# Optimization experiments

Hardware: AMD Instinct MI355X
Metric: run time of the kernel (lower is better)

The kernel has to match this reference:

```python
import jax, jax.numpy as jnp
import numpy as np

T, NTOK, D = 8, 32768, 128
N_ENTIRE, COMP_LEN, COMP_DIM = 65536, 8, 64


def _layer_norm(v, w, b, eps=1e-5):
    m = v.mean(-1, keepdims=True)
    c = v - m
    var = (c * c).mean(-1, keepdims=True)
    return c * jax.lax.rsqrt(var + eps) * w + b


def setup_inputs() -> dict:
    key = jax.random.key(0)
    ks = jax.random.split(key, 8)
    x = jax.random.normal(ks[0], (T, NTOK, D), jnp.float32)
    padded_node_mask = jnp.ones((T, NTOK), dtype=bool)  # all tokens are nodes
    # unique per-timestamp scatter indices into the 'entire node' axis
    node_idx = jax.vmap(lambda k: jax.random.permutation(k, N_ENTIRE)[:NTOK])(
        jax.random.split(ks[1], T)).astype(jnp.int32)
    s = 0.02
    return dict(
        x=x,
        ln1_w=jnp.ones((D,), jnp.float32), ln1_b=jnp.zeros((D,), jnp.float32),
        w1=jax.random.normal(ks[2], (D, 2 * COMP_DIM), jnp.float32) * s,
        b1=jnp.zeros((2 * COMP_DIM,), jnp.float32),
        w2=jax.random.normal(ks[3], (2 * COMP_DIM, COMP_DIM), jnp.float32) * s,
        b2=jnp.zeros((COMP_DIM,), jnp.float32),
        lnf_w=jnp.ones((COMP_LEN * COMP_DIM,), jnp.float32),
        lnf_b=jnp.zeros((COMP_LEN * COMP_DIM,), jnp.float32),
        padded_node_mask=padded_node_mask,
        node_idx=node_idx,
        n_entire=N_ENTIRE,
    )


def reference(x, ln1_w, ln1_b, w1, b1, w2, b2, lnf_w, lnf_b,
              padded_node_mask, node_idx, n_entire):
    t, ntok, d = x.shape
    # encode_layer_norm over all tokens
    xn = _layer_norm(x, ln1_w, ln1_b)
    # nodes = xn[padded_node_mask].reshape(t, ntok, d); mask is all-True here
    nodes = jnp.where(padded_node_mask[..., None], xn, 0.0)
    # scga._to_entire: scatter nodes into [t, n_entire, d] (zeros elsewhere)
    tenodes = jnp.zeros((t, n_entire, d), x.dtype)
    tenodes = tenodes.at[jnp.arange(t)[:, None], node_idx].set(nodes)
    # eval mode: np.array_split(arange(n_entire), comp_len) = equal contiguous groups
    g = n_entire // COMP_LEN
    xg = tenodes.reshape(t, COMP_LEN, g, d)  # [t, L, g, d]
    # per-group MLP (Linear->GELU->(Dropout=id)->Linear) then mean over group
    h = jax.nn.gelu(jnp.einsum('tlgd,de->tlge', xg, w1) + b1, approximate=False)
    c = jnp.einsum('tlge,ec->tlgc', h, w2) + b2
    comp = c.mean(axis=2)  # [t, L, comp_dim]
    compressed = _layer_norm(comp.reshape(t, 1, COMP_LEN * COMP_DIM), lnf_w, lnf_b)
    # orthogonality loss over the L compressed components (exact torch pair loop)
    f = comp.transpose(1, 0, 2).reshape(COMP_LEN, -1)  # [L, t*comp_dim]
    fn = f / jnp.linalg.norm(f, axis=-1, keepdims=True)
    dots = []
    for i in range(COMP_LEN - 1):
        for j in range(1, COMP_LEN):
            dots.append(jnp.sum(fn[i] * fn[j]) / jnp.sum(fn[i] + fn[j]))
    ortho_loss = jnp.mean(jnp.stack(dots) ** 2)
    return compressed, ortho_loss
```

## Files before the change

### kernel.cpp

```cpp
#include <hip/hip_runtime.h>
#include <math.h>

#define TT 8
#define NTOK 32768
#define DD 128
#define LCOMP 8
#define GSZ 8192
#define CDIM 64
#define EDIM 128
#define NPART 32

#define TOKB 64
#define NBLK (TT*NTOK/TOKB)

#define O_CZERO 0
#define O_W2BT  256
#define O_W1BT  (256 + EDIM*CDIM*2)
#define O_CSUMP (O_W1BT + DD*EDIM*2)

typedef __attribute__((ext_vector_type(8))) short bf16x8;
typedef __attribute__((ext_vector_type(4))) float f32x4;

__device__ __forceinline__ ushort f2bf(float f) {
    union { float f; uint u; } c; c.f = f;
    uint u = c.u;
    return (ushort)((u + 0x7FFFu + ((u >> 16) & 1u)) >> 16);
}

__device__ __forceinline__ float gelu_f(float a) {
    float x = a * 0.70710678118654752f;
    float ax = fabsf(x);
    float t = 1.0f / (1.0f + 0.3275911f * ax);
    float p = t * (0.254829592f + t * (-0.284496736f + t * (1.421413741f +
              t * (-1.453152027f + t * 1.061405429f))));
    float e = __expf(-x * x);
    float er = copysignf(1.0f - p * e, x);
    return 0.5f * a * (1.0f + er);
}

__device__ __forceinline__ void gl_lds16(const void* g, void* l) {
    __builtin_amdgcn_global_load_lds(
        (const __attribute__((address_space(1))) void*)g,
        (__attribute__((address_space(3))) void*)l, 16, 0, 0);
}

__global__ void prep_kernel(const float* __restrict__ w1, const float* __restrict__ b1,
                            const float* __restrict__ w2,
                            ushort* __restrict__ w1bt, ushort* __restrict__ w2bt,
                            float* __restrict__ czero) {
    int gid = blockIdx.x * 256 + threadIdx.x;
    if (gid < DD * EDIM) {
        int j = gid >> 7, d = gid & 127;
        int slot = (d >> 3) ^ (j & 7);
        w1bt[j * 128 + slot * 8 + (d & 7)] = f2bf(w1[d * EDIM + j]);
    }
    if (gid < EDIM * CDIM) {
        int k = gid >> 7, jj = gid & 127;
        w2bt[k * 128 + jj] = f2bf(w2[jj * CDIM + k]);
    }
    if (gid < CDIM) {
        float a2 = 0.f;
        for (int dd = 0; dd < EDIM; ++dd)
            a2 += gelu_f(b1[dd]) * w2[dd * CDIM + gid];
        czero[gid] = a2;
    }
}

__global__ __launch_bounds__(256, 2)
void main_kernel(const float* __restrict__ x,
                 const float* __restrict__ ln1w, const float* __restrict__ ln1b,
                 const float* __restrict__ b1g,
                 const ushort* __restrict__ w1bt, const ushort* __restrict__ w2bt,
                 const float* __restrict__ czero,
                 const int* __restrict__ node_idx,
                 float* __restrict__ csum_p) {
    __shared__ float  s_x[TOKB * DD];
    __shared__ ushort s_w1[DD * EDIM];
    __shared__ float  s_acc[LCOMP * CDIM];
    __shared__ int    s_l[TOKB];

    const int tid = threadIdx.x;
    const int w   = tid >> 6;
    const int ln  = tid & 63;
    const int bid = blockIdx.x;
    const size_t tokbase = (size_t)bid * TOKB;

    bf16x8 b2f[4][4];
#pragma unroll
    for (int kt = 0; kt < 4; ++kt)
#pragma unroll
        for (int ks = 0; ks < 4; ++ks) {
            int krow = kt * 16 + (ln & 15);
            b2f[kt][ks] = *(const bf16x8*)(w2bt + krow * EDIM + ks * 32 + (ln >> 4) * 8);
        }

    s_acc[tid] = 0.f; s_acc[tid + 256] = 0.f;
    if (tid < TOKB) s_l[tid] = node_idx[tokbase + tid] >> 13;

    {
        const char* xg = (const char*)(x + tokbase * DD);
        const char* wg = (const char*)w1bt;
        char* lx = (char*)s_x;
        char* lw = (char*)s_w1;
#pragma unroll
        for (int sx = 0; sx < 8; ++sx) {
            int off  = (w * 8 + sx) * 1024 + ln * 16;
            int row  = off >> 9;
            int slot = (off >> 4) & 31;
            int sc   = slot ^ (row & 7);
            gl_lds16(xg + row * 512 + sc * 16, lx + off);
            gl_lds16(wg + off, lw + off);
        }
    }
    __syncthreads();

    const int row = w * 16 + (ln & 15);
    const int cs  = ln >> 4;
    float v[32];
#pragma unroll
    for (int sx = 0; sx < 8; ++sx) {
        int slot = (cs * 8 + sx) ^ (row & 7);
        float4 f = *(const float4*)((const char*)s_x + row * 512 + slot * 16);
        v[sx*4+0]=f.x; v[sx*4+1]=f.y; v[sx*4+2]=f.z; v[sx*4+3]=f.w;
    }
    {
        float s = 0.f, q = 0.f;
#pragma unroll
        for (int i2 = 0; i2 < 32; ++i2) { s += v[i2]; q += v[i2]*v[i2]; }
        s += __shfl_xor(s, 16, 64); q += __shfl_xor(q, 16, 64);
        s += __shfl_xor(s, 32, 64); q += __shfl_xor(q, 32, 64);
        float m   = s * (1.f/128.f);
        float var = q * (1.f/128.f) - m*m;
        float rs  = rsqrtf(var + 1e-5f);
#pragma unroll
        for (int sx = 0; sx < 8; ++sx) {
            float4 w4 = *(const float4*)(ln1w + cs*32 + sx*4);
            float4 b4 = *(const float4*)(ln1b + cs*32 + sx*4);
            v[sx*4+0] = (v[sx*4+0]-m)*rs*w4.x + b4.x;
            v[sx*4+1] = (v[sx*4+1]-m)*rs*w4.y + b4.y;
            v[sx*4+2] = (v[sx*4+2]-m)*rs*w4.z + b4.z;
            v[sx*4+3] = (v[sx*4+3]-m)*rs*w4.w + b4.w;
        }
    }

    bf16x8 b1f[2][4];
#pragma unroll
    for (int jt = 0; jt < 2; ++jt)
#pragma unroll
        for (int ks = 0; ks < 4; ++ks) {
            int jrow = w * 32 + jt * 16 + (ln & 15);
            int slot = (ks * 4 + (ln >> 4)) ^ (jrow & 7);
            b1f[jt][ks] = *(const bf16x8*)((const char*)s_w1 + jrow * 256 + slot * 16);
        }
    float b1v0 = b1g[w * 32 + (ln & 15)];
    float b1v1 = b1g[w * 32 + 16 + (ln & 15)];

    __syncthreads();

    ushort* xn = (ushort*)s_x;
    ushort* hb = (ushort*)s_x + TOKB*DD;
#pragma unroll
    for (int u = 0; u < 4; ++u) {
        uint4 pk;
        pk.x = f2bf(v[u*8+0]) | ((uint)f2bf(v[u*8+1]) << 16);
        pk.y = f2bf(v[u*8+2]) | ((uint)f2bf(v[u*8+3]) << 16);
        pk.z = f2bf(v[u*8+4]) | ((uint)f2bf(v[u*8+5]) << 16);
        pk.w = f2bf(v[u*8+6]) | ((uint)f2bf(v[u*8+7]) << 16);
        int slot = (cs * 4 + u) ^ (row & 7);
        *(uint4*)((char*)xn + row * 256 + slot * 16) = pk;
    }
    __syncthreads();

#pragma unroll
    for (int tt = 0; tt < 4; ++tt) {
        bf16x8 a4[4];
        int ar = tt * 16 + (ln & 15);
#pragma unroll
        for (int ks = 0; ks < 4; ++ks) {
            int slot = (ks * 4 + (ln >> 4)) ^ (ar & 7);
            a4[ks] = *(const bf16x8*)((const char*)xn + ar * 256 + slot * 16);
        }
        f32x4 ac0 = {0.f,0.f,0.f,0.f}, ac1 = {0.f,0.f,0.f,0.f};
#pragma unroll
        for (int ks = 0; ks < 4; ++ks) {
            ac0 = __builtin_amdgcn_mfma_f32_16x16x32_bf16(a4[ks], b1f[0][ks], ac0, 0, 0, 0);
            ac1 = __builtin_amdgcn_mfma_f32_16x16x32_bf16(a4[ks], b1f[1][ks], ac1, 0, 0, 0);
        }
        int hrb = tt * 16 + (ln >> 4) * 4;
        int j0  = w * 32 + (ln & 15);
        int j1  = j0 + 16;
#pragma unroll
        for (int r = 0; r < 4; ++r) {
            float h0 = gelu_f(ac0[r] + b1v0);
            float h1 = gelu_f(ac1[r] + b1v1);
            int hrow = hrb + r;
            int sl0 = (j0 >> 3) ^ (hrow & 7);
            int sl1 = (j1 >> 3) ^ (hrow & 7);
            *(ushort*)((char*)hb + hrow*256 + sl0*16 + (j0 & 7)*2) = f2bf(h0);
            *(ushort*)((char*)hb + hrow*256 + sl1*16 + (j1 & 7)*2) = f2bf(h1);
        }
    }
    __syncthreads();

    {
        bf16x8 a4[4];
        int ar = w * 16 + (ln & 15);
#pragma unroll
        for (int ks = 0; ks < 4; ++ks) {
            int slot = (ks * 4 + (ln >> 4)) ^ (ar & 7);
            a4[ks] = *(const bf16x8*)((const char*)hb + ar * 256 + slot * 16);
        }
        f32x4 acc0 = {0.f,0.f,0.f,0.f}, acc1 = {0.f,0.f,0.f,0.f};
        f32x4 acc2 = {0.f,0.f,0.f,0.f}, acc3 = {0.f,0.f,0.f,0.f};
#pragma unroll
        for (int ks = 0; ks < 4; ++ks) {
            acc0 = __builtin_amdgcn_mfma_f32_16x16x32_bf16(a4[ks], b2f[0][ks], acc0, 0, 0, 0);
            acc1 = __builtin_amdgcn_mfma_f32_16x16x32_bf16(a4[ks], b2f[1][ks], acc1, 0, 0, 0);
            acc2 = __builtin_amdgcn_mfma_f32_16x16x32_bf16(a4[ks], b2f[2][ks], acc2, 0, 0, 0);
            acc3 = __builtin_amdgcn_mfma_f32_16x16x32_bf16(a4[ks], b2f[3][ks], acc3, 0, 0, 0);
        }
        int tok0 = w * 16 + (ln >> 4) * 4;
        int l0 = s_l[tok0+0], l1 = s_l[tok0+1], l2 = s_l[tok0+2], l3 = s_l[tok0+3];
#pragma unroll
        for (int kt = 0; kt < 4; ++kt) {
            f32x4 a = (kt==0)?acc0:(kt==1)?acc1:(kt==2)?acc2:acc3;
            int k = kt * 16 + (ln & 15);
            float czk = czero[k];
            atomicAdd(&s_acc[l0 * CDIM + k], a[0] - czk);
            atomicAdd(&s_acc[l1 * CDIM + k], a[1] - czk);
            atomicAdd(&s_acc[l2 * CDIM + k], a[2] - czk);
            atomicAdd(&s_acc[l3 * CDIM + k], a[3] - czk);
        }
    }
    __syncthreads();

    {
        int t8 = (bid >> 9) * LCOMP;
        int p  = bid & (NPART - 1);
#pragma unroll
        for (int i2 = 0; i2 < 2; ++i2) {
            int idx = tid + i2 * 256;
            int l = idx >> 6, k = idx & 63;
            atomicAdd(&csum_p[(p * 64 + t8 + l) * 64 + k], s_acc[idx]);
        }
    }
}

__global__ void fin_kernel(const float* __restrict__ csum_p, const float* __restrict__ czero,
                           const float* __restrict__ b2,
                           const float* __restrict__ lnfw, const float* __restrict__ lnfb,
                           float* __restrict__ out) {
    __shared__ float comp[TT * LCOMP * CDIM];
    __shared__ float norm_s[LCOMP], sum_s[LCOMP], red[8];
    int tid = threadIdx.x;

    for (int idx = tid; idx < TT * LCOMP * CDIM; idx += 512) {
        int bin = idx >> 6, k = idx & 63;
        float s = 0.f;
        for (int p = 0; p < NPART; ++p) s += csum_p[(p * 64 + bin) * 64 + k];
        comp[idx] = s * (1.f / GSZ) + czero[k] + b2[k];
    }
    __syncthreads();

    int wave = tid >> 6, lane = tid & 63;

    {
        int t = wave;
        float s = 0.f, q = 0.f;
        for (int e = lane; e < 512; e += 64) {
            float v = comp[t * 512 + e];
            s += v; q += v * v;
        }
#pragma unroll
        for (int off = 32; off > 0; off >>= 1) {
            s += __shfl_xor(s, off, 64);
            q += __shfl_xor(q, off, 64);
        }
        float m = s * (1.f / 512.f);
        float var = q * (1.f / 512.f) - m * m;
        float rs = rsqrtf(var + 1e-5f);
        for (int e = lane; e < 512; e += 64) {
            float v = comp[t * 512 + e];
            out[t * 512 + e] = (v - m) * rs * lnfw[e] + lnfb[e];
        }
    }

    {
        int l = wave;
        float s2 = 0.f, s1 = 0.f;
        for (int qd = lane; qd < 512; qd += 64) {
            int t = qd >> 6, k = qd & 63;
            float v = comp[t * 512 + l * 64 + k];
            s2 += v * v; s1 += v;
        }
#pragma unroll
        for (int off = 32; off > 0; off >>= 1) {
            s2 += __shfl_xor(s2, off, 64);
            s1 += __shfl_xor(s1, off, 64);
        }
        if (lane == 0) { norm_s[l] = sqrtf(s2); sum_s[l] = s1; }
    }
    __syncthreads();

    float loss_part = 0.f;
    for (int p = wave; p < 49; p += 8) {
        int i = p / 7, j = 1 + p % 7;
        float d = 0.f;
        for (int qd = lane; qd < 512; qd += 64) {
            int t = qd >> 6, k = qd & 63;
            d += comp[t * 512 + i * 64 + k] * comp[t * 512 + j * 64 + k];
        }
#pragma unroll
        for (int off = 32; off > 0; off >>= 1) d += __shfl_xor(d, off, 64);
        float ni = norm_s[i], nj = norm_s[j];
        float dot = (d / (ni * nj)) / (sum_s[i] / ni + sum_s[j] / nj);
        loss_part += dot * dot;
    }
    if (lane == 0) red[wave] = loss_part;
    __syncthreads();
    if (tid == 0) {
        float tot = 0.f;
        for (int w2_ = 0; w2_ < 8; ++w2_) tot += red[w2_];
        out[4096] = tot * (1.f / 49.f);
    }
}

extern "C" void kernel_launch(void* const* d_in, const int* in_sizes, int n_in,
                              void* d_out, int out_size, void* d_ws, size_t ws_size,
                              hipStream_t stream) {
    const float* x    = (const float*)d_in[0];
    const float* ln1w = (const float*)d_in[1];
    const float* ln1b = (const float*)d_in[2];
    const float* w1   = (const float*)d_in[3];
    const float* b1   = (const float*)d_in[4];
    const float* w2   = (const float*)d_in[5];
    const float* b2   = (const float*)d_in[6];
    const float* lnfw = (const float*)d_in[7];
    const float* lnfb = (const float*)d_in[8];
    const int* node_idx = (const int*)d_in[10];
    float* out = (float*)d_out;

    char* wsb = (char*)d_ws;
    float*  czero = (float*)(wsb + O_CZERO);
    ushort* w2bt  = (ushort*)(wsb + O_W2BT);
    ushort* w1bt  = (ushort*)(wsb + O_W1BT);
    float*  csum_p = (float*)(wsb + O_CSUMP);

    hipMemsetAsync(csum_p, 0, NPART * 64 * 64 * sizeof(float), stream);
    prep_kernel<<<64, 256, 0, stream>>>(w1, b1, w2, w1bt, w2bt, czero);
    main_kernel<<<NBLK, 256, 0, stream>>>(x, ln1w, ln1b, b1, w1bt, w2bt, czero,
                                          node_idx, csum_p);
    fin_kernel<<<1, 512, 0, stream>>>(csum_p, czero, b2, lnfw, lnfb, out);
}
```

Measured before the change: 351.0 us.

## Make main kernel persistent over four token tiles with register prefetch

Each block now processes four 64-token tiles in a loop. The next tile's x is loaded into registers while the current tile's MLP runs, replacing the async global-to-LDS copy. The W1 tile staged in LDS is dropped; W1 and W2 fragments are read straight from global/L2 each tile, and launch bounds rise to 4 blocks per CU. The memset is folded into the prep kernel. Together these aim to amortise per-block setup, overlap loads with compute, raise occupancy and remove one launch, at the cost of repeated weight reads and less inter-block parallelism.

```diff
diff --git a/kernel.cpp b/kernel.cpp
--- a/kernel.cpp
+++ b/kernel.cpp
@@ -11,7 +11,8 @@
 #define NPART 32
 
 #define TOKB 64
-#define NBLK (TT*NTOK/TOKB)
+#define TILES 4
+#define NBLK (TT*NTOK/(TOKB*TILES))
 
 #define O_CZERO 0
 #define O_W2BT  256
@@ -38,16 +39,10 @@
     return 0.5f * a * (1.0f + er);
 }
 
-__device__ __forceinline__ void gl_lds16(const void* g, void* l) {
-    __builtin_amdgcn_global_load_lds(
-        (const __attribute__((address_space(1))) void*)g,
-        (__attribute__((address_space(3))) void*)l, 16, 0, 0);
-}
-
 __global__ void prep_kernel(const float* __restrict__ w1, const float* __restrict__ b1,
                             const float* __restrict__ w2,
                             ushort* __restrict__ w1bt, ushort* __restrict__ w2bt,
-                            float* __restrict__ czero) {
+                            float* __restrict__ czero, float* __restrict__ csum_p) {
     int gid = blockIdx.x * 256 + threadIdx.x;
     if (gid < DD * EDIM) {
         int j = gid >> 7, d = gid & 127;
@@ -64,9 +59,12 @@
             a2 += gelu_f(b1[dd]) * w2[dd * CDIM + gid];
         czero[gid] = a2;
     }
-}
-
-__global__ __launch_bounds__(256, 2)
+#pragma unroll
+    for (int i = 0; i < 8; ++i)
+        csum_p[gid + i * 16384] = 0.f;
+}
+
+__global__ __launch_bounds__(256, 4)
 void main_kernel(const float* __restrict__ x,
                  const float* __restrict__ ln1w, const float* __restrict__ ln1b,
                  const float* __restrict__ b1g,
@@ -74,168 +72,152 @@
                  const float* __restrict__ czero,
                  const int* __restrict__ node_idx,
                  float* __restrict__ csum_p) {
-    __shared__ float  s_x[TOKB * DD];
-    __shared__ ushort s_w1[DD * EDIM];
+    __shared__ ushort s_xn[TOKB * DD];
+    __shared__ ushort s_h[TOKB * DD];
     __shared__ float  s_acc[LCOMP * CDIM];
-    __shared__ int    s_l[TOKB];
 
     const int tid = threadIdx.x;
     const int w   = tid >> 6;
     const int ln  = tid & 63;
+    const int cs  = ln >> 4;
+    const int row = w * 16 + (ln & 15);
     const int bid = blockIdx.x;
-    const size_t tokbase = (size_t)bid * TOKB;
-
-    bf16x8 b2f[4][4];
-#pragma unroll
-    for (int kt = 0; kt < 4; ++kt)
-#pragma unroll
-        for (int ks = 0; ks < 4; ++ks) {
-            int krow = kt * 16 + (ln & 15);
-            b2f[kt][ks] = *(const bf16x8*)(w2bt + krow * EDIM + ks * 32 + (ln >> 4) * 8);
-        }
+    const size_t base0 = (size_t)bid * (TOKB * TILES);
 
     s_acc[tid] = 0.f; s_acc[tid + 256] = 0.f;
-    if (tid < TOKB) s_l[tid] = node_idx[tokbase + tid] >> 13;
-
+
+    const float b1v0 = b1g[w * 32 + (ln & 15)];
+    const float b1v1 = b1g[w * 32 + 16 + (ln & 15)];
+    float czv[4];
+#pragma unroll
+    for (int kt = 0; kt < 4; ++kt) czv[kt] = czero[kt * 16 + (ln & 15)];
+
+    float v[32];
     {
-        const char* xg = (const char*)(x + tokbase * DD);
-        const char* wg = (const char*)w1bt;
-        char* lx = (char*)s_x;
-        char* lw = (char*)s_w1;
+        const float* xp = x + (base0 + row) * DD + cs * 32;
 #pragma unroll
         for (int sx = 0; sx < 8; ++sx) {
-            int off  = (w * 8 + sx) * 1024 + ln * 16;
-            int row  = off >> 9;
-            int slot = (off >> 4) & 31;
-            int sc   = slot ^ (row & 7);
-            gl_lds16(xg + row * 512 + sc * 16, lx + off);
-            gl_lds16(wg + off, lw + off);
-        }
-    }
-    __syncthreads();
-
-    const int row = w * 16 + (ln & 15);
-    const int cs  = ln >> 4;
-    float v[32];
-#pragma unroll
-    for (int sx = 0; sx < 8; ++sx) {
-        int slot = (cs * 8 + sx) ^ (row & 7);
-        float4 f = *(const float4*)((const char*)s_x + row * 512 + slot * 16);
-        v[sx*4+0]=f.x; v[sx*4+1]=f.y; v[sx*4+2]=f.z; v[sx*4+3]=f.w;
-    }
+            float4 f = *(const float4*)(xp + sx * 4);
+            v[sx*4+0]=f.x; v[sx*4+1]=f.y; v[sx*4+2]=f.z; v[sx*4+3]=f.w;
+        }
+    }
+
+    for (int tile = 0; tile < TILES; ++tile) {
+        {
+            float s = 0.f, q = 0.f;
+#pragma unroll
+            for (int i2 = 0; i2 < 32; ++i2) { s += v[i2]; q += v[i2]*v[i2]; }
+            s += __shfl_xor(s, 16, 64); q += __shfl_xor(q, 16, 64);
+            s += __shfl_xor(s, 32, 64); q += __shfl_xor(q, 32, 64);
+            float m   = s * (1.f/128.f);
+            float var = q * (1.f/128.f) - m*m;
+            float rs  = rsqrtf(var + 1e-5f);
+#pragma unroll
+            for (int sx = 0; sx < 8; ++sx) {
+                float4 w4 = *(const float4*)(ln1w + cs*32 + sx*4);
+                float4 b4 = *(const float4*)(ln1b + cs*32 + sx*4);
+                v[sx*4+0] = (v[sx*4+0]-m)*rs*w4.x + b4.x;
+                v[sx*4+1] = (v[sx*4+1]-m)*rs*w4.y + b4.y;
+                v[sx*4+2] = (v[sx*4+2]-m)*rs*w4.z + b4.z;
+                v[sx*4+3] = (v[sx*4+3]-m)*rs*w4.w + b4.w;
+            }
+        }
+#pragma unroll
+        for (int u = 0; u < 4; ++u) {
+            uint4 pk;
+            pk.x = f2bf(v[u*8+0]) | ((uint)f2bf(v[u*8+1]) << 16);
+            pk.y = f2bf(v[u*8+2]) | ((uint)f2bf(v[u*8+3]) << 16);
+            pk.z = f2bf(v[u*8+4]) | ((uint)f2bf(v[u*8+5]) << 16);
+            pk.w = f2bf(v[u*8+6]) | ((uint)f2bf(v[u*8+7]) << 16);
+            int slot = (cs * 4 + u) ^ (row & 7);
+            *(uint4*)((char*)s_xn + row * 256 + slot * 16) = pk;
+        }
+        __syncthreads();
+
+        if (tile + 1 < TILES) {
+            const float* xp = x + (base0 + (tile + 1) * TOKB + row) * DD + cs * 32;
+#pragma unroll
+            for (int sx = 0; sx < 8; ++sx) {
+                float4 f = *(const float4*)(xp + sx * 4);
+                v[sx*4+0]=f.x; v[sx*4+1]=f.y; v[sx*4+2]=f.z; v[sx*4+3]=f.w;
+            }
+        }
+
+        bf16x8 b1f[2][4];
+#pragma unroll
+        for (int jt = 0; jt < 2; ++jt)
+#pragma unroll
+            for (int ks = 0; ks < 4; ++ks) {
+                int jrow = w * 32 + jt * 16 + (ln & 15);
+                int slot = (ks * 4 + cs) ^ (jrow & 7);
+                b1f[jt][ks] = *(const bf16x8*)((const char*)w1bt + jrow * 256 + slot * 16);
+            }
+#pragma unroll
+        for (int tt = 0; tt < 4; ++tt) {
+            bf16x8 a4[4];
+            int ar = tt * 16 + (ln & 15);
+#pragma unroll
+            for (int ks = 0; ks < 4; ++ks) {
+                int slot = (ks * 4 + cs) ^ (ar & 7);
+                a4[ks] = *(const bf16x8*)((const char*)s_xn + ar * 256 + slot * 16);
+            }
+            f32x4 ac0 = {0.f,0.f,0.f,0.f}, ac1 = {0.f,0.f,0.f,0.f};
+#pragma unroll
+            for (int ks = 0; ks < 4; ++ks) {
+                ac0 = __builtin_amdgcn_mfma_f32_16x16x32_bf16(a4[ks], b1f[0][ks], ac0, 0, 0, 0);
+                ac1 = __builtin_amdgcn_mfma_f32_16x16x32_bf16(a4[ks], b1f[1][ks], ac1, 0, 0, 0);
+            }
+            int hrb = tt * 16 + cs * 4;
+            int j0  = w * 32 + (ln & 15);
+            int j1  = j0 + 16;
+#pragma unroll
+            for (int r = 0; r < 4; ++r) {
+                float h0 = gelu_f(ac0[r] + b1v0);
+                float h1 = gelu_f(ac1[r] + b1v1);
+                int hrow = hrb + r;
+                int sl0 = (j0 >> 3) ^ (hrow & 7);
+                int sl1 = (j1 >> 3) ^ (hrow & 7);
+                *(ushort*)((char*)s_h + hrow*256 + sl0*16 + (j0 & 7)*2) = f2bf(h0);
+                *(ushort*)((char*)s_h + hrow*256 + sl1*16 + (j1 & 7)*2) = f2bf(h1);
+            }
+        }
+        __syncthreads();
+
+        {
+            bf16x8 a4[4];
+            int ar = w * 16 + (ln & 15);
+#pragma unroll
+            for (int ks = 0; ks < 4; ++ks) {
+                int slot = (ks * 4 + cs) ^ (ar & 7);
+                a4[ks] = *(const bf16x8*)((const char*)s_h + ar * 256 + slot * 16);
+            }
+            int tok0 = w * 16 + cs * 4;
+            int4 li = *(const int4*)(node_idx + base0 + (size_t)tile * TOKB + tok0);
+            int l0 = li.x >> 13, l1 = li.y >> 13, l2 = li.z >> 13, l3 = li.w >> 13;
+#pragma unroll
+            for (int kt = 0; kt < 4; ++kt) {
+                bf16x8 bfr[4];
+                int krow = kt * 16 + (ln & 15);
+#pragma unroll
+                for (int ks = 0; ks < 4; ++ks)
+                    bfr[ks] = *(const bf16x8*)(w2bt + krow * EDIM + ks * 32 + cs * 8);
+                f32x4 acc = {0.f,0.f,0.f,0.f};
+#pragma unroll
+                for (int ks = 0; ks < 4; ++ks)
+                    acc = __builtin_amdgcn_mfma_f32_16x16x32_bf16(a4[ks], bfr[ks], acc, 0, 0, 0);
+                int k = kt * 16 + (ln & 15);
+                float czk = czv[kt];
+                atomicAdd(&s_acc[l0 * CDIM + k], acc[0] - czk);
+                atomicAdd(&s_acc[l1 * CDIM + k], acc[1] - czk);
+                atomicAdd(&s_acc[l2 * CDIM + k], acc[2] - czk);
+                atomicAdd(&s_acc[l3 * CDIM + k], acc[3] - czk);
+            }
+        }
+        __syncthreads();
+    }
+
     {
-        float s = 0.f, q = 0.f;
-#pragma unroll
-        for (int i2 = 0; i2 < 32; ++i2) { s += v[i2]; q += v[i2]*v[i2]; }
-        s += __shfl_xor(s, 16, 64); q += __shfl_xor(q, 16, 64);
-        s += __shfl_xor(s, 32, 64); q += __shfl_xor(q, 32, 64);
-        float m   = s * (1.f/128.f);
-        float var = q * (1.f/128.f) - m*m;
-        float rs  = rsqrtf(var + 1e-5f);
-#pragma unroll
-        for (int sx = 0; sx < 8; ++sx) {
-            float4 w4 = *(const float4*)(ln1w + cs*32 + sx*4);
-            float4 b4 = *(const float4*)(ln1b + cs*32 + sx*4);
-            v[sx*4+0] = (v[sx*4+0]-m)*rs*w4.x + b4.x;
-            v[sx*4+1] = (v[sx*4+1]-m)*rs*w4.y + b4.y;
-            v[sx*4+2] = (v[sx*4+2]-m)*rs*w4.z + b4.z;
-            v[sx*4+3] = (v[sx*4+3]-m)*rs*w4.w + b4.w;
-        }
-    }
-
-    bf16x8 b1f[2][4];
-#pragma unroll
-    for (int jt = 0; jt < 2; ++jt)
-#pragma unroll
-        for (int ks = 0; ks < 4; ++ks) {
-            int jrow = w * 32 + jt * 16 + (ln & 15);
-            int slot = (ks * 4 + (ln >> 4)) ^ (jrow & 7);
-            b1f[jt][ks] = *(const bf16x8*)((const char*)s_w1 + jrow * 256 + slot * 16);
-        }
-    float b1v0 = b1g[w * 32 + (ln & 15)];
-    float b1v1 = b1g[w * 32 + 16 + (ln & 15)];
-
-    __syncthreads();
-
-    ushort* xn = (ushort*)s_x;
-    ushort* hb = (ushort*)s_x + TOKB*DD;
-#pragma unroll
-    for (int u = 0; u < 4; ++u) {
-        uint4 pk;
-        pk.x = f2bf(v[u*8+0]) | ((uint)f2bf(v[u*8+1]) << 16);
-        pk.y = f2bf(v[u*8+2]) | ((uint)f2bf(v[u*8+3]) << 16);
-        pk.z = f2bf(v[u*8+4]) | ((uint)f2bf(v[u*8+5]) << 16);
-        pk.w = f2bf(v[u*8+6]) | ((uint)f2bf(v[u*8+7]) << 16);
-        int slot = (cs * 4 + u) ^ (row & 7);
-        *(uint4*)((char*)xn + row * 256 + slot * 16) = pk;
-    }
-    __syncthreads();
-
-#pragma unroll
-    for (int tt = 0; tt < 4; ++tt) {
-        bf16x8 a4[4];
-        int ar = tt * 16 + (ln & 15);
-#pragma unroll
-        for (int ks = 0; ks < 4; ++ks) {
-            int slot = (ks * 4 + (ln >> 4)) ^ (ar & 7);
-            a4[ks] = *(const bf16x8*)((const char*)xn + ar * 256 + slot * 16);
-        }
-        f32x4 ac0 = {0.f,0.f,0.f,0.f}, ac1 = {0.f,0.f,0.f,0.f};
-#pragma unroll
-        for (int ks = 0; ks < 4; ++ks) {
-            ac0 = __builtin_amdgcn_mfma_f32_16x16x32_bf16(a4[ks], b1f[0][ks], ac0, 0, 0, 0);
-            ac1 = __builtin_amdgcn_mfma_f32_16x16x32_bf16(a4[ks], b1f[1][ks], ac1, 0, 0, 0);
-        }
-        int hrb = tt * 16 + (ln >> 4) * 4;
-        int j0  = w * 32 + (ln & 15);
-        int j1  = j0 + 16;
-#pragma unroll
-        for (int r = 0; r < 4; ++r) {
-            float h0 = gelu_f(ac0[r] + b1v0);
-            float h1 = gelu_f(ac1[r] + b1v1);
-            int hrow = hrb + r;
-            int sl0 = (j0 >> 3) ^ (hrow & 7);
-            int sl1 = (j1 >> 3) ^ (hrow & 7);
-            *(ushort*)((char*)hb + hrow*256 + sl0*16 + (j0 & 7)*2) = f2bf(h0);
-            *(ushort*)((char*)hb + hrow*256 + sl1*16 + (j1 & 7)*2) = f2bf(h1);
-        }
-    }
-    __syncthreads();
-
-    {
-        bf16x8 a4[4];
-        int ar = w * 16 + (ln & 15);
-#pragma unroll
-        for (int ks = 0; ks < 4; ++ks) {
-            int slot = (ks * 4 + (ln >> 4)) ^ (ar & 7);
-            a4[ks] = *(const bf16x8*)((const char*)hb + ar * 256 + slot * 16);
-        }
-        f32x4 acc0 = {0.f,0.f,0.f,0.f}, acc1 = {0.f,0.f,0.f,0.f};
-        f32x4 acc2 = {0.f,0.f,0.f,0.f}, acc3 = {0.f,0.f,0.f,0.f};
-#pragma unroll
-        for (int ks = 0; ks < 4; ++ks) {
-            acc0 = __builtin_amdgcn_mfma_f32_16x16x32_bf16(a4[ks], b2f[0][ks], acc0, 0, 0, 0);
-            acc1 = __builtin_amdgcn_mfma_f32_16x16x32_bf16(a4[ks], b2f[1][ks], acc1, 0, 0, 0);
-            acc2 = __builtin_amdgcn_mfma_f32_16x16x32_bf16(a4[ks], b2f[2][ks], acc2, 0, 0, 0);
-            acc3 = __builtin_amdgcn_mfma_f32_16x16x32_bf16(a4[ks], b2f[3][ks], acc3, 0, 0, 0);
-        }
-        int tok0 = w * 16 + (ln >> 4) * 4;
-        int l0 = s_l[tok0+0], l1 = s_l[tok0+1], l2 = s_l[tok0+2], l3 = s_l[tok0+3];
-#pragma unroll
-        for (int kt = 0; kt < 4; ++kt) {
-            f32x4 a = (kt==0)?acc0:(kt==1)?acc1:(kt==2)?acc2:acc3;
-            int k = kt * 16 + (ln & 15);
-            float czk = czero[k];
-            atomicAdd(&s_acc[l0 * CDIM + k], a[0] - czk);
-            atomicAdd(&s_acc[l1 * CDIM + k], a[1] - czk);
-            atomicAdd(&s_acc[l2 * CDIM + k], a[2] - czk);
-            atomicAdd(&s_acc[l3 * CDIM + k], a[3] - czk);
-        }
-    }
-    __syncthreads();
-
-    {
-        int t8 = (bid >> 9) * LCOMP;
+        int t8 = (bid >> 7) * LCOMP;
         int p  = bid & (NPART - 1);
 #pragma unroll
         for (int i2 = 0; i2 < 2; ++i2) {
@@ -341,13 +323,12 @@
     float* out = (float*)d_out;
 
     char* wsb = (char*)d_ws;
-    float*  czero = (float*)(wsb + O_CZERO);
-    ushort* w2bt  = (ushort*)(wsb + O_W2BT);
-    ushort* w1bt  = (ushort*)(wsb + O_W1BT);
+    float*  czero  = (float*)(wsb + O_CZERO);
+    ushort* w2bt   = (ushort*)(wsb + O_W2BT);
+    ushort* w1bt   = (ushort*)(wsb + O_W1BT);
     float*  csum_p = (float*)(wsb + O_CSUMP);
 
-    hipMemsetAsync(csum_p, 0, NPART * 64 * 64 * sizeof(float), stream);
-    prep_kernel<<<64, 256, 0, stream>>>(w1, b1, w2, w1bt, w2bt, czero);
+    prep_kernel<<<64, 256, 0, stream>>>(w1, b1, w2, w1bt, w2bt, czero, csum_p);
     main_kernel<<<NBLK, 256, 0, stream>>>(x, ln1w, ln1b, b1, w1bt, w2bt, czero,
                                           node_idx, csum_p);
     fin_kernel<<<1, 512, 0, stream>>>(csum_p, czero, b2, lnfw, lnfb, out);
```

After: 422.4 us. 20.3% more time.
